# Kernel tuning notes

Measured on AMD Instinct MI355X. Metric: run time of the kernel, lower is better.

Reference implementation:

```python
import jax, jax.numpy as jnp
import numpy as np

B, N, F_IN, F_OUT = 8, 2048, 256, 64
ALPHA = 0.2          # LeakyReLU negative slope
NEG_INF = -9e15      # matches -9000000000000000.0 in the torch code


def setup_inputs() -> dict:
    key = jax.random.key(0)
    k = jax.random.split(key, 7)
    x = jax.random.normal(k[0], (B, N, F_IN), dtype=jnp.float32)
    adj = jax.random.randint(k[1], (B, N, N), 0, 2, dtype=jnp.int32)
    # W: nn.Linear(in_features, out_features)
    W = jax.random.normal(k[2], (F_IN, F_OUT), dtype=jnp.float32) / np.sqrt(F_IN)
    b_W = jax.random.normal(k[3], (F_OUT,), dtype=jnp.float32) * 0.01
    # a: nn.Linear(2*out_features, 1); decomposed as a_src (first F_OUT rows,
    # multiplies h_i) and a_dst (last F_OUT rows, multiplies h_j) + bias.
    a_src = jax.random.normal(k[4], (F_OUT,), dtype=jnp.float32) / np.sqrt(2 * F_OUT)
    a_dst = jax.random.normal(k[5], (F_OUT,), dtype=jnp.float32) / np.sqrt(2 * F_OUT)
    a_b = jax.random.normal(k[6], (), dtype=jnp.float32) * 0.01
    return {"x": x, "adj": adj, "W": W, "b_W": b_W,
            "a_src": a_src, "a_dst": a_dst, "a_b": a_b}


def reference(x, adj, W, b_W, a_src, a_dst, a_b):
    # h = W(input): [B, N, F_OUT]
    h = jnp.einsum('bnf,fo->bno', x, W) + b_W
    # Additive attention decomposition: a([h_i || h_j]) = a_src.h_i + a_dst.h_j + b
    # (avoids materializing the [B, N, N, 2F] concat tensor of the original)
    src = jnp.einsum('bno,o->bn', h, a_src)  # row term  (h_i)
    dst = jnp.einsum('bno,o->bn', h, a_dst)  # col term  (h_j)
    e = jax.nn.leaky_relu(src[:, :, None] + dst[:, None, :] + a_b, ALPHA)  # [B,N,N]
    e = jnp.where(adj > 0, e, NEG_INF)
    attention = jax.nn.softmax(e, axis=2)
    h_prime = jnp.einsum('bij,bjo->bio', attention, h)  # [B, N, F_OUT]
    return jax.nn.elu(h_prime)  # concat=True branch
```

## Files before the change

kernel.cpp:

```cpp
#include <hip/hip_runtime.h>

#define B_   8
#define N_   2048
#define FIN  256
#define FOUT 64
#define ALPHA 0.2f

typedef __attribute__((ext_vector_type(8))) short bf16x8;
typedef __attribute__((ext_vector_type(8))) unsigned short u16x8;
typedef __attribute__((ext_vector_type(4))) float f32x4;

__device__ __forceinline__ float b2f(unsigned short u) {
    union { unsigned int u; float f; } v; v.u = ((unsigned int)u) << 16; return v.f;
}
__device__ __forceinline__ unsigned short f2b(float f) {
    union { float f; unsigned int u; } v; v.f = f;
    unsigned int r = v.u + 0x7FFFu + ((v.u >> 16) & 1u);
    return (unsigned short)(r >> 16);
}

__global__ __launch_bounds__(256) void k_hgemm(
    const float* __restrict__ x, const float* __restrict__ W,
    const float* __restrict__ bW, unsigned short* __restrict__ h)
{
    const int tid = threadIdx.x;
    const int wv = tid >> 6, lane = tid & 63;
    const int quad = lane >> 4, col = lane & 15;
    const int f = wv * 16 + col;

    bf16x8 Bf[8];
    #pragma unroll
    for (int kk = 0; kk < 8; ++kk) {
        bf16x8 t;
        #pragma unroll
        for (int j = 0; j < 8; ++j)
            t[j] = (short)f2b(W[(kk * 32 + quad * 8 + j) * FOUT + f]);
        Bf[kk] = t;
    }
    const float bias = bW[f];
    const int rowbase = blockIdx.x * 64;
    #pragma unroll
    for (int rt = 0; rt < 4; ++rt) {
        const int r0 = rowbase + rt * 16;
        f32x4 acc = {0.f, 0.f, 0.f, 0.f};
        #pragma unroll
        for (int kk = 0; kk < 8; ++kk) {
            const float* xp = x + (size_t)(r0 + col) * FIN + kk * 32 + quad * 8;
            float4 x0 = *(const float4*)xp;
            float4 x1 = *(const float4*)(xp + 4);
            bf16x8 Af;
            Af[0] = (short)f2b(x0.x); Af[1] = (short)f2b(x0.y);
            Af[2] = (short)f2b(x0.z); Af[3] = (short)f2b(x0.w);
            Af[4] = (short)f2b(x1.x); Af[5] = (short)f2b(x1.y);
            Af[6] = (short)f2b(x1.z); Af[7] = (short)f2b(x1.w);
            acc = __builtin_amdgcn_mfma_f32_16x16x32_bf16(Af, Bf[kk], acc, 0, 0, 0);
        }
        #pragma unroll
        for (int reg = 0; reg < 4; ++reg) {
            int r = r0 + quad * 4 + reg;
            h[(size_t)r * FOUT + f] = f2b(acc[reg] + bias);
        }
    }
}

__global__ __launch_bounds__(256) void k_tr_srcdst(
    const unsigned short* __restrict__ h,
    const float* __restrict__ asrc, const float* __restrict__ adst,
    unsigned short* __restrict__ hT, float* __restrict__ src, float* __restrict__ dst)
{
    __shared__ float as_s[FOUT], ad_s[FOUT];
    __shared__ unsigned short tileT[FOUT * 72];
    const int tid = threadIdx.x;
    if (tid < FOUT) { as_s[tid] = asrc[tid]; ad_s[tid] = adst[tid]; }
    __syncthreads();
    const int r0 = blockIdx.x * 64;
    const int b = r0 >> 11;
    const int j0b = r0 & (N_ - 1);
    {
        const int i = tid >> 2, fb = (tid & 3) * 16;
        const unsigned short* hp = h + (size_t)(r0 + i) * FOUT + fb;
        u16x8 v0 = *(const u16x8*)hp;
        u16x8 v1 = *(const u16x8*)(hp + 8);
        float sp = 0.f, dp = 0.f;
        #pragma unroll
        for (int k = 0; k < 8; ++k) {
            float hv = b2f(v0[k]);
            sp += hv * as_s[fb + k]; dp += hv * ad_s[fb + k];
            tileT[(fb + k) * 72 + i] = v0[k];
        }
        #pragma unroll
        for (int k = 0; k < 8; ++k) {
            float hv = b2f(v1[k]);
            sp += hv * as_s[fb + 8 + k]; dp += hv * ad_s[fb + 8 + k];
            tileT[(fb + 8 + k) * 72 + i] = v1[k];
        }
        sp += __shfl_xor(sp, 1); sp += __shfl_xor(sp, 2);
        dp += __shfl_xor(dp, 1); dp += __shfl_xor(dp, 2);
        if ((tid & 3) == 0) { src[r0 + i] = sp; dst[r0 + i] = dp; }
    }
    __syncthreads();
    {
        const int fq = tid >> 2, ic = (tid & 3) * 16;
        u16x8 o0 = *(const u16x8*)&tileT[fq * 72 + ic];
        u16x8 o1 = *(const u16x8*)&tileT[fq * 72 + ic + 8];
        unsigned short* op = hT + (size_t)(b * FOUT + fq) * N_ + j0b + ic;
        *(u16x8*)op = o0;
        *(u16x8*)(op + 8) = o1;
    }
}

__global__ __launch_bounds__(256) void k_attn(
    const int* __restrict__ adj, const float* __restrict__ src, const float* __restrict__ dst,
    const unsigned short* __restrict__ hT, const float* __restrict__ abp,
    float* __restrict__ out)
{
    __shared__ unsigned short h_s[2][64 * 136];
    __shared__ unsigned short w_s[2][32 * 136];
    __shared__ float src_s[32];
    __shared__ float l_s[32];

    const int tid = threadIdx.x;
    const int wv = tid >> 6, lane = tid & 63;
    const int quad = lane >> 4, col = lane & 15;
    const int b = blockIdx.x >> 6;
    const int i0 = (blockIdx.x & 63) * 32;

    if (tid < 32) src_s[tid] = src[b * N_ + i0 + tid];
    __syncthreads();

    const int il = tid >> 3, jg = tid & 7;
    const float srci = src_s[il] + abp[0];
    const int fq = tid >> 2, q4 = tid & 3;
    const unsigned short* hTbase = hT + (size_t)(b * FOUT + fq) * N_ + q4 * 32;
    const int* adjbase = adj + (size_t)(b * N_ + i0 + il) * N_ + jg * 16;
    const float* dstbase = dst + b * N_ + jg * 16;

    u16x8 hv0 = *(const u16x8*)(hTbase);
    u16x8 hv1 = *(const u16x8*)(hTbase + 8);
    u16x8 hv2 = *(const u16x8*)(hTbase + 16);
    u16x8 hv3 = *(const u16x8*)(hTbase + 24);
    int4 a0 = *(const int4*)(adjbase);
    int4 a1 = *(const int4*)(adjbase + 4);
    int4 a2 = *(const int4*)(adjbase + 8);
    int4 a3 = *(const int4*)(adjbase + 12);
    float4 d0 = *(const float4*)(dstbase);
    float4 d1 = *(const float4*)(dstbase + 4);
    float4 d2 = *(const float4*)(dstbase + 8);
    float4 d3 = *(const float4*)(dstbase + 12);

    float lsum = 0.f;
    f32x4 acc0 = {0, 0, 0, 0}, acc1 = {0, 0, 0, 0};

    for (int jt = 0; jt < 16; ++jt) {
        const int buf = jt & 1;
        {
            unsigned short* q = &h_s[buf][fq * 136 + q4 * 32];
            *(u16x8*)q = hv0; *(u16x8*)(q + 8) = hv1;
            *(u16x8*)(q + 16) = hv2; *(u16x8*)(q + 24) = hv3;
        }
        {
            int av[16] = {a0.x, a0.y, a0.z, a0.w, a1.x, a1.y, a1.z, a1.w,
                          a2.x, a2.y, a2.z, a2.w, a3.x, a3.y, a3.z, a3.w};
            float dv[16] = {d0.x, d0.y, d0.z, d0.w, d1.x, d1.y, d1.z, d1.w,
                            d2.x, d2.y, d2.z, d2.w, d3.x, d3.y, d3.z, d3.w};
            u16x8 p0, p1;
            float ls = 0.f;
            #pragma unroll
            for (int k = 0; k < 16; ++k) {
                float e = srci + dv[k];
                e = e > 0.f ? e : ALPHA * e;
                float wval = av[k] > 0 ? __expf(e) : 0.f;
                unsigned short wb = f2b(wval);
                ls += b2f(wb);
                if (k < 8) p0[k] = wb; else p1[k - 8] = wb;
            }
            lsum += ls;
            unsigned short* q = &w_s[buf][il * 136 + jg * 16];
            *(u16x8*)q = p0; *(u16x8*)(q + 8) = p1;
        }
        __syncthreads();
        {
            const int jn = (jt < 15) ? (jt + 1) * 128 : 0;
            hv0 = *(const u16x8*)(hTbase + jn);
            hv1 = *(const u16x8*)(hTbase + jn + 8);
            hv2 = *(const u16x8*)(hTbase + jn + 16);
            hv3 = *(const u16x8*)(hTbase + jn + 24);
            a0 = *(const int4*)(adjbase + jn);
            a1 = *(const int4*)(adjbase + jn + 4);
            a2 = *(const int4*)(adjbase + jn + 8);
            a3 = *(const int4*)(adjbase + jn + 12);
            d0 = *(const float4*)(dstbase + jn);
            d1 = *(const float4*)(dstbase + jn + 4);
            d2 = *(const float4*)(dstbase + jn + 8);
            d3 = *(const float4*)(dstbase + jn + 12);
        }
        {
            #pragma unroll
            for (int kk = 0; kk < 4; ++kk) {
                bf16x8 A0 = *(const bf16x8*)&w_s[buf][col * 136 + kk * 32 + quad * 8];
                bf16x8 A1 = *(const bf16x8*)&w_s[buf][(16 + col) * 136 + kk * 32 + quad * 8];
                bf16x8 Bf = *(const bf16x8*)&h_s[buf][(wv * 16 + col) * 136 + kk * 32 + quad * 8];
                acc0 = __builtin_amdgcn_mfma_f32_16x16x32_bf16(A0, Bf, acc0, 0, 0, 0);
                acc1 = __builtin_amdgcn_mfma_f32_16x16x32_bf16(A1, Bf, acc1, 0, 0, 0);
            }
        }
    }

    lsum += __shfl_xor(lsum, 1);
    lsum += __shfl_xor(lsum, 2);
    lsum += __shfl_xor(lsum, 4);
    if (jg == 0) l_s[il] = lsum;
    __syncthreads();

    #pragma unroll
    for (int m = 0; m < 2; ++m) {
        f32x4 a = m ? acc1 : acc0;
        #pragma unroll
        for (int reg = 0; reg < 4; ++reg) {
            int row = m * 16 + quad * 4 + reg;
            float l = l_s[row];
            l = l > 0.f ? l : 1.f;
            float v = a[reg] / l;
            v = v > 0.f ? v : (__expf(v) - 1.f);
            out[(size_t)(b * N_ + i0 + row) * FOUT + wv * 16 + col] = v;
        }
    }
}

extern "C" void kernel_launch(void* const* d_in, const int* in_sizes, int n_in,
                              void* d_out, int out_size, void* d_ws, size_t ws_size,
                              hipStream_t stream)
{
    const float* x    = (const float*)d_in[0];
    const int*   adj  = (const int*)d_in[1];
    const float* W    = (const float*)d_in[2];
    const float* bW   = (const float*)d_in[3];
    const float* asrc = (const float*)d_in[4];
    const float* adst = (const float*)d_in[5];
    const float* abp  = (const float*)d_in[6];
    float* out = (float*)d_out;

    char* ws = (char*)d_ws;
    unsigned short* h  = (unsigned short*)ws;
    unsigned short* hT = (unsigned short*)(ws + (size_t)2 * 1024 * 1024);
    float* src = (float*)(ws + (size_t)4 * 1024 * 1024);
    float* dst = (float*)(ws + (size_t)4 * 1024 * 1024 + 64 * 1024);

    k_hgemm<<<256, 256, 0, stream>>>(x, W, bW, h);
    k_tr_srcdst<<<256, 256, 0, stream>>>(h, asrc, adst, hT, src, dst);
    k_attn<<<512, 256, 0, stream>>>(adj, src, dst, hT, abp, out);
}
```

Before: 222.8 us.

## Fuse h GEMM with transpose/score kernel and halve attention row tile

Merges the projection GEMM with the transpose and src/dst score computation, so h goes straight into a shared-memory tile and the intermediate h buffer and one launch are removed. The attention kernel now handles 16 query rows per block instead of 32, doubling the grid to 1024 blocks for more parallelism. In exchange, each block reloads the full hT for its batch, so hT traffic doubles, and each block issues half as many MFMAs per shared-memory h tile.

```diff
diff --git a/kernel.cpp b/kernel.cpp
--- a/kernel.cpp
+++ b/kernel.cpp
@@ -19,15 +19,22 @@
     return (unsigned short)(r >> 16);
 }
 
-__global__ __launch_bounds__(256) void k_hgemm(
+__global__ __launch_bounds__(256) void k_hgemm_tr(
     const float* __restrict__ x, const float* __restrict__ W,
-    const float* __restrict__ bW, unsigned short* __restrict__ h)
+    const float* __restrict__ bW, const float* __restrict__ asrc,
+    const float* __restrict__ adst,
+    unsigned short* __restrict__ hT, float* __restrict__ src, float* __restrict__ dst)
 {
+    __shared__ unsigned short tileT[FOUT * 72];
+    __shared__ float as_s[FOUT], ad_s[FOUT];
+
     const int tid = threadIdx.x;
     const int wv = tid >> 6, lane = tid & 63;
     const int quad = lane >> 4, col = lane & 15;
     const int f = wv * 16 + col;
 
+    if (tid < FOUT) { as_s[tid] = asrc[tid]; ad_s[tid] = adst[tid]; }
+
     bf16x8 Bf[8];
     #pragma unroll
     for (int kk = 0; kk < 8; ++kk) {
@@ -38,14 +45,17 @@
         Bf[kk] = t;
     }
     const float bias = bW[f];
-    const int rowbase = blockIdx.x * 64;
+    const int r0 = blockIdx.x * 64;
+    const int b = r0 >> 11;
+    const int j0b = r0 & (N_ - 1);
+
     #pragma unroll
     for (int rt = 0; rt < 4; ++rt) {
-        const int r0 = rowbase + rt * 16;
+        const int rr = r0 + rt * 16;
         f32x4 acc = {0.f, 0.f, 0.f, 0.f};
         #pragma unroll
         for (int kk = 0; kk < 8; ++kk) {
-            const float* xp = x + (size_t)(r0 + col) * FIN + kk * 32 + quad * 8;
+            const float* xp = x + (size_t)(rr + col) * FIN + kk * 32 + quad * 8;
             float4 x0 = *(const float4*)xp;
             float4 x1 = *(const float4*)(xp + 4);
             bf16x8 Af;
@@ -57,48 +67,24 @@
         }
         #pragma unroll
         for (int reg = 0; reg < 4; ++reg) {
-            int r = r0 + quad * 4 + reg;
-            h[(size_t)r * FOUT + f] = f2b(acc[reg] + bias);
-        }
-    }
-}
-
-__global__ __launch_bounds__(256) void k_tr_srcdst(
-    const unsigned short* __restrict__ h,
-    const float* __restrict__ asrc, const float* __restrict__ adst,
-    unsigned short* __restrict__ hT, float* __restrict__ src, float* __restrict__ dst)
-{
-    __shared__ float as_s[FOUT], ad_s[FOUT];
-    __shared__ unsigned short tileT[FOUT * 72];
-    const int tid = threadIdx.x;
-    if (tid < FOUT) { as_s[tid] = asrc[tid]; ad_s[tid] = adst[tid]; }
+            int row = rt * 16 + quad * 4 + reg;
+            tileT[f * 72 + row] = f2b(acc[reg] + bias);
+        }
+    }
     __syncthreads();
-    const int r0 = blockIdx.x * 64;
-    const int b = r0 >> 11;
-    const int j0b = r0 & (N_ - 1);
+
     {
         const int i = tid >> 2, fb = (tid & 3) * 16;
-        const unsigned short* hp = h + (size_t)(r0 + i) * FOUT + fb;
-        u16x8 v0 = *(const u16x8*)hp;
-        u16x8 v1 = *(const u16x8*)(hp + 8);
         float sp = 0.f, dp = 0.f;
         #pragma unroll
-        for (int k = 0; k < 8; ++k) {
-            float hv = b2f(v0[k]);
+        for (int k = 0; k < 16; ++k) {
+            float hv = b2f(tileT[(fb + k) * 72 + i]);
             sp += hv * as_s[fb + k]; dp += hv * ad_s[fb + k];
-            tileT[(fb + k) * 72 + i] = v0[k];
-        }
-        #pragma unroll
-        for (int k = 0; k < 8; ++k) {
-            float hv = b2f(v1[k]);
-            sp += hv * as_s[fb + 8 + k]; dp += hv * ad_s[fb + 8 + k];
-            tileT[(fb + 8 + k) * 72 + i] = v1[k];
         }
         sp += __shfl_xor(sp, 1); sp += __shfl_xor(sp, 2);
         dp += __shfl_xor(dp, 1); dp += __shfl_xor(dp, 2);
         if ((tid & 3) == 0) { src[r0 + i] = sp; dst[r0 + i] = dp; }
     }
-    __syncthreads();
     {
         const int fq = tid >> 2, ic = (tid & 3) * 16;
         u16x8 o0 = *(const u16x8*)&tileT[fq * 72 + ic];
@@ -115,25 +101,25 @@
     float* __restrict__ out)
 {
     __shared__ unsigned short h_s[2][64 * 136];
-    __shared__ unsigned short w_s[2][32 * 136];
-    __shared__ float src_s[32];
-    __shared__ float l_s[32];
+    __shared__ unsigned short w_s[2][16 * 136];
+    __shared__ float src_s[16];
+    __shared__ float l_s[16];
 
     const int tid = threadIdx.x;
     const int wv = tid >> 6, lane = tid & 63;
     const int quad = lane >> 4, col = lane & 15;
-    const int b = blockIdx.x >> 6;
-    const int i0 = (blockIdx.x & 63) * 32;
-
-    if (tid < 32) src_s[tid] = src[b * N_ + i0 + tid];
+    const int b = blockIdx.x >> 7;
+    const int i0 = (blockIdx.x & 127) * 16;
+
+    if (tid < 16) src_s[tid] = src[b * N_ + i0 + tid];
     __syncthreads();
 
-    const int il = tid >> 3, jg = tid & 7;
+    const int il = tid >> 4, jg = tid & 15;
     const float srci = src_s[il] + abp[0];
     const int fq = tid >> 2, q4 = tid & 3;
     const unsigned short* hTbase = hT + (size_t)(b * FOUT + fq) * N_ + q4 * 32;
-    const int* adjbase = adj + (size_t)(b * N_ + i0 + il) * N_ + jg * 16;
-    const float* dstbase = dst + b * N_ + jg * 16;
+    const int* adjbase = adj + (size_t)(b * N_ + i0 + il) * N_ + jg * 8;
+    const float* dstbase = dst + b * N_ + jg * 8;
 
     u16x8 hv0 = *(const u16x8*)(hTbase);
     u16x8 hv1 = *(const u16x8*)(hTbase + 8);
@@ -141,15 +127,11 @@
     u16x8 hv3 = *(const u16x8*)(hTbase + 24);
     int4 a0 = *(const int4*)(adjbase);
     int4 a1 = *(const int4*)(adjbase + 4);
-    int4 a2 = *(const int4*)(adjbase + 8);
-    int4 a3 = *(const int4*)(adjbase + 12);
     float4 d0 = *(const float4*)(dstbase);
     float4 d1 = *(const float4*)(dstbase + 4);
-    float4 d2 = *(const float4*)(dstbase + 8);
-    float4 d3 = *(const float4*)(dstbase + 12);
 
     float lsum = 0.f;
-    f32x4 acc0 = {0, 0, 0, 0}, acc1 = {0, 0, 0, 0};
+    f32x4 acc0 = {0, 0, 0, 0};
 
     for (int jt = 0; jt < 16; ++jt) {
         const int buf = jt & 1;
@@ -159,49 +141,40 @@
             *(u16x8*)(q + 16) = hv2; *(u16x8*)(q + 24) = hv3;
         }
         {
-            int av[16] = {a0.x, a0.y, a0.z, a0.w, a1.x, a1.y, a1.z, a1.w,
-                          a2.x, a2.y, a2.z, a2.w, a3.x, a3.y, a3.z, a3.w};
-            float dv[16] = {d0.x, d0.y, d0.z, d0.w, d1.x, d1.y, d1.z, d1.w,
-                            d2.x, d2.y, d2.z, d2.w, d3.x, d3.y, d3.z, d3.w};
-            u16x8 p0, p1;
+            int av[8] = {a0.x, a0.y, a0.z, a0.w, a1.x, a1.y, a1.z, a1.w};
+            float dv[8] = {d0.x, d0.y, d0.z, d0.w, d1.x, d1.y, d1.z, d1.w};
+            u16x8 p0;
             float ls = 0.f;
             #pragma unroll
-            for (int k = 0; k < 16; ++k) {
+            for (int k = 0; k < 8; ++k) {
                 float e = srci + dv[k];
                 e = e > 0.f ? e : ALPHA * e;
                 float wval = av[k] > 0 ? __expf(e) : 0.f;
                 unsigned short wb = f2b(wval);
                 ls += b2f(wb);
-                if (k < 8) p0[k] = wb; else p1[k - 8] = wb;
+                p0[k] = wb;
             }
             lsum += ls;
-            unsigned short* q = &w_s[buf][il * 136 + jg * 16];
-            *(u16x8*)q = p0; *(u16x8*)(q + 8) = p1;
+            *(u16x8*)&w_s[buf][il * 136 + jg * 8] = p0;
         }
         __syncthreads();
         {
-            const int jn = (jt < 15) ? (jt + 1) * 128 : 0;
+            const int jn = ((jt + 1) & 15) * 128;
             hv0 = *(const u16x8*)(hTbase + jn);
             hv1 = *(const u16x8*)(hTbase + jn + 8);
             hv2 = *(const u16x8*)(hTbase + jn + 16);
             hv3 = *(const u16x8*)(hTbase + jn + 24);
             a0 = *(const int4*)(adjbase + jn);
             a1 = *(const int4*)(adjbase + jn + 4);
-            a2 = *(const int4*)(adjbase + jn + 8);
-            a3 = *(const int4*)(adjbase + jn + 12);
             d0 = *(const float4*)(dstbase + jn);
             d1 = *(const float4*)(dstbase + jn + 4);
-            d2 = *(const float4*)(dstbase + jn + 8);
-            d3 = *(const float4*)(dstbase + jn + 12);
         }
         {
             #pragma unroll
             for (int kk = 0; kk < 4; ++kk) {
                 bf16x8 A0 = *(const bf16x8*)&w_s[buf][col * 136 + kk * 32 + quad * 8];
-                bf16x8 A1 = *(const bf16x8*)&w_s[buf][(16 + col) * 136 + kk * 32 + quad * 8];
                 bf16x8 Bf = *(const bf16x8*)&h_s[buf][(wv * 16 + col) * 136 + kk * 32 + quad * 8];
                 acc0 = __builtin_amdgcn_mfma_f32_16x16x32_bf16(A0, Bf, acc0, 0, 0, 0);
-                acc1 = __builtin_amdgcn_mfma_f32_16x16x32_bf16(A1, Bf, acc1, 0, 0, 0);
             }
         }
     }
@@ -209,21 +182,18 @@
     lsum += __shfl_xor(lsum, 1);
     lsum += __shfl_xor(lsum, 2);
     lsum += __shfl_xor(lsum, 4);
+    lsum += __shfl_xor(lsum, 8);
     if (jg == 0) l_s[il] = lsum;
     __syncthreads();
 
     #pragma unroll
-    for (int m = 0; m < 2; ++m) {
-        f32x4 a = m ? acc1 : acc0;
-        #pragma unroll
-        for (int reg = 0; reg < 4; ++reg) {
-            int row = m * 16 + quad * 4 + reg;
-            float l = l_s[row];
-            l = l > 0.f ? l : 1.f;
-            float v = a[reg] / l;
-            v = v > 0.f ? v : (__expf(v) - 1.f);
-            out[(size_t)(b * N_ + i0 + row) * FOUT + wv * 16 + col] = v;
-        }
+    for (int reg = 0; reg < 4; ++reg) {
+        int row = quad * 4 + reg;
+        float l = l_s[row];
+        l = l > 0.f ? l : 1.f;
+        float v = acc0[reg] / l;
+        v = v > 0.f ? v : (__expf(v) - 1.f);
+        out[(size_t)(b * N_ + i0 + row) * FOUT + wv * 16 + col] = v;
     }
 }
 
@@ -241,12 +211,10 @@
     float* out = (float*)d_out;
 
     char* ws = (char*)d_ws;
-    unsigned short* h  = (unsigned short*)ws;
-    unsigned short* hT = (unsigned short*)(ws + (size_t)2 * 1024 * 1024);
-    float* src = (float*)(ws + (size_t)4 * 1024 * 1024);
-    float* dst = (float*)(ws + (size_t)4 * 1024 * 1024 + 64 * 1024);
-
-    k_hgemm<<<256, 256, 0, stream>>>(x, W, bW, h);
-    k_tr_srcdst<<<256, 256, 0, stream>>>(h, asrc, adst, hT, src, dst);
-    k_attn<<<512, 256, 0, stream>>>(adj, src, dst, hT, abp, out);
-}
+    unsigned short* hT = (unsigned short*)ws;
+    float* src = (float*)(ws + (size_t)2 * 1024 * 1024);
+    float* dst = (float*)(ws + (size_t)2 * 1024 * 1024 + 64 * 1024);
+
+    k_hgemm_tr<<<256, 256, 0, stream>>>(x, W, bW, asrc, adst, hT, src, dst);
+    k_attn<<<1024, 256, 0, stream>>>(adj, src, dst, hT, abp, out);
+}
```

Result: slower. 233.6 us (+4.9%).
